# Kernel tuning notes

Measured on AMD Instinct MI355X. Metric: run time of the kernel, lower is better.

The kernel has to match this reference:

```python
import jax, jax.numpy as jnp
import numpy as np

H = 10        # hidden_size
N_TASKS = 5
N_STEPS = 10


def setup_inputs() -> dict:
    key = jax.random.key(0)
    ks = jax.random.split(key, 10)
    omega = jnp.array([0.2, 0.4, 0.6, 0.8, 1.0], dtype=jnp.float32)
    # per-(task, step) human noise: torch.randn(1) * 0.05 each call
    noise = jax.random.normal(ks[0], (N_TASKS, N_STEPS), dtype=jnp.float32) * 0.05
    # h_go1 = randint(0,4,4), h_go2 = randint(4,8,4) -> timestep membership masks
    go1_idx = jax.random.randint(ks[1], (4,), 0, 4)
    go2_idx = jax.random.randint(ks[2], (4,), 4, 8)
    go1_mask = jnp.zeros(N_STEPS, dtype=bool).at[go1_idx].set(True)
    go2_mask = jnp.zeros(N_STEPS, dtype=bool).at[go2_idx].set(True)

    def p(k, shape, fan_in):
        return jax.random.normal(k, shape, dtype=jnp.float32) / jnp.sqrt(jnp.float32(fan_in))

    W_ih = p(ks[3], (4 * H, 2), 2)      # LSTM input weights (gate order i,f,g,o)
    W_hh = p(ks[4], (4 * H, H), H)      # LSTM recurrent weights
    b_ih = p(ks[5], (4 * H,), H)
    b_hh = p(ks[6], (4 * H,), H)
    w1 = p(ks[7], (2 * H, H), H)
    b1 = jnp.zeros(2 * H, jnp.float32)
    w2 = p(ks[8], (2 * H, 2 * H), 2 * H)
    b2 = jnp.zeros(2 * H, jnp.float32)
    w3 = p(ks[9], (1, 2 * H), 2 * H)
    b3 = jnp.zeros(1, jnp.float32)
    return dict(omega=omega, noise=noise, go1_mask=go1_mask, go2_mask=go2_mask,
                W_ih=W_ih, W_hh=W_hh, b_ih=b_ih, b_hh=b_hh,
                w1=w1, b1=b1, w2=w2, b2=b2, w3=w3, b3=b3)


def reference(omega, noise, go1_mask, go2_mask, W_ih, W_hh, b_ih, b_hh,
              w1, b1, w2, b2, w3, b3):
    # human(): branch on s_star in {0.4, 0.8} -> go1 / scale 0.2, else go2 / scale 0.4
    is_g1 = jnp.isclose(omega, 0.4) | jnp.isclose(omega, 0.8)          # [T]
    scale = jnp.where(is_g1, 0.2, 0.4)                                  # [T]
    tmask = jnp.where(is_g1[:, None], go1_mask[None, :], go2_mask[None, :])  # [T,S]
    ah = jnp.where(tmask, (omega - 0.6)[:, None] / scale[:, None], 0.0) + noise  # [T,S]

    def step(carry, ah_t):
        s, h, c, err = carry                       # s:[T], h,c:[T,H], err:[T]
        x = jnp.stack([s, ah_t], axis=-1)          # context = cat(s, ah) -> [T,2]
        gates = x @ W_ih.T + h @ W_hh.T + (b_ih + b_hh)   # [T,4H]
        i, f, g, o = jnp.split(gates, 4, axis=-1)
        i = jax.nn.sigmoid(i); f = jax.nn.sigmoid(f)
        g = jnp.tanh(g);       o = jax.nn.sigmoid(o)
        c = f * c + i * g
        h = o * jnp.tanh(c)
        h1 = jax.nn.relu(h @ w1.T + b1)
        h2 = jax.nn.relu(h1 @ w2.T + b2)
        ar = (h2 @ w3.T + b3)[:, 0]                # robot action [T]
        s = s + ar
        err = err + (s - omega) ** 2
        return (s, h, c, err), None

    init = (jnp.zeros(N_TASKS, jnp.float32),
            jnp.zeros((N_TASKS, H), jnp.float32),
            jnp.zeros((N_TASKS, H), jnp.float32),
            jnp.zeros(N_TASKS, jnp.float32))
    (s, h, c, err), _ = jax.lax.scan(step, init, ah.T)   # scan over the 10 steps
    return jnp.sum(err)    # Q = sum over the 5 tasks of per-rollout squared error
```

## Files before the change

kernel.cpp:

```cpp
#include <hip/hip_runtime.h>

#define HID 10
#define NT 5
#define NS 10

__device__ __forceinline__ float sigf(float x) {
    return 1.0f / (1.0f + __expf(-x));
}
__device__ __forceinline__ float tanh_fast(float x) {
    return 2.0f / (1.0f + __expf(-2.0f * x)) - 1.0f;
}

__device__ __forceinline__ unsigned decode_mask(const void* p) {
    const unsigned* pu = (const unsigned*)p;
    const unsigned char* pb = (const unsigned char*)p;
    unsigned mi = 0, mf = 0, mb = 0;
    bool oki = true, okf = true;
#pragma unroll
    for (int i = 0; i < NS; ++i) {
        unsigned v = pu[i];
        if (v == 1u) mi |= (1u << i);
        else if (v != 0u) oki = false;
        if (v == 0x3F800000u) mf |= (1u << i);
        else if (v != 0u) okf = false;
        if (pb[i]) mb |= (1u << i);
    }
    return oki ? mi : (okf ? mf : mb);
}

__global__ __launch_bounds__(64, 1) void rnnae_kernel(
    const float* __restrict__ omega, const float* __restrict__ noise,
    const void* __restrict__ go1, const void* __restrict__ go2,
    const float* __restrict__ W_ih, const float* __restrict__ W_hh,
    const float* __restrict__ b_ih, const float* __restrict__ b_hh,
    const float* __restrict__ w1, const float* __restrict__ b1,
    const float* __restrict__ w2, const float* __restrict__ b2,
    const float* __restrict__ w3, const float* __restrict__ b3,
    float* __restrict__ out)
{
    const int lane = (int)threadIdx.x;
    float err = 0.0f;

    if (lane < NT * HID) {
        const int t = lane / HID;
        const int u = lane - t * HID;
        const int grp = t * HID;

        const unsigned m1 = decode_mask(go1);
        const unsigned m2 = decode_mask(go2);

        const float om = omega[t];
        const bool is_g1 = (fabsf(om - 0.4f) < 1e-4f) || (fabsf(om - 0.8f) < 1e-4f);
        const float scale = is_g1 ? 0.2f : 0.4f;
        const unsigned msk = is_g1 ? m1 : m2;
        const float base = (om - 0.6f) / scale;

        float ah[NS];
#pragma unroll
        for (int st = 0; st < NS; ++st)
            ah[st] = (((msk >> st) & 1u) ? base : 0.0f) + noise[t * NS + st];

        float wih0[4], wih1[4], whh[4][HID], bg[4];
#pragma unroll
        for (int g = 0; g < 4; ++g) {
            const int r = g * HID + u;
            wih0[g] = W_ih[r * 2 + 0];
            wih1[g] = W_ih[r * 2 + 1];
            bg[g]   = b_ih[r] + b_hh[r];
#pragma unroll
            for (int j = 0; j < HID; ++j) whh[g][j] = W_hh[r * HID + j];
        }
        float w1a[HID], w1b[HID];
#pragma unroll
        for (int j = 0; j < HID; ++j) {
            w1a[j] = w1[u * HID + j];
            w1b[j] = w1[(u + HID) * HID + j];
        }
        const float b1a = b1[u], b1b = b1[u + HID];
        float w2a[2 * HID], w2b[2 * HID];
#pragma unroll
        for (int k = 0; k < 2 * HID; ++k) {
            w2a[k] = w2[u * 2 * HID + k];
            w2b[k] = w2[(u + HID) * 2 * HID + k];
        }
        const float b2a = b2[u], b2b = b2[u + HID];
        const float w3u  = w3[u];
        const float w3uh = w3[u + HID];
        const float b3v  = b3[0];

        float s = 0.0f, c = 0.0f;
        float hj[HID];
#pragma unroll
        for (int j = 0; j < HID; ++j) hj[j] = 0.0f;

#pragma unroll
        for (int st = 0; st < NS; ++st) {
            float acc[4];
#pragma unroll
            for (int g = 0; g < 4; ++g) {
                float a = bg[g] + wih0[g] * s + wih1[g] * ah[st];
#pragma unroll
                for (int j = 0; j < HID; ++j) a += whh[g][j] * hj[j];
                acc[g] = a;
            }
            const float ig = sigf(acc[0]);
            const float fg = sigf(acc[1]);
            const float gg = tanh_fast(acc[2]);
            const float og = sigf(acc[3]);
            c = fg * c + ig * gg;
            const float h = og * tanh_fast(c);

#pragma unroll
            for (int j = 0; j < HID; ++j) hj[j] = __shfl(h, grp + j);

            float x1a = b1a, x1b = b1b;
#pragma unroll
            for (int j = 0; j < HID; ++j) {
                x1a += w1a[j] * hj[j];
                x1b += w1b[j] * hj[j];
            }
            const float h1a = fmaxf(x1a, 0.0f);
            const float h1b = fmaxf(x1b, 0.0f);

            float h1v[2 * HID];
#pragma unroll
            for (int j = 0; j < HID; ++j) {
                h1v[j]       = __shfl(h1a, grp + j);
                h1v[j + HID] = __shfl(h1b, grp + j);
            }
            float x2a = b2a, x2b = b2b;
#pragma unroll
            for (int k = 0; k < 2 * HID; ++k) {
                x2a += w2a[k] * h1v[k];
                x2b += w2b[k] * h1v[k];
            }
            const float h2a = fmaxf(x2a, 0.0f);
            const float h2b = fmaxf(x2b, 0.0f);

            const float pa = w3u * h2a + w3uh * h2b;
            float ar = b3v;
#pragma unroll
            for (int j = 0; j < HID; ++j) ar += __shfl(pa, grp + j);

            s += ar;
            const float d = s - om;
            err += d * d;
        }
    }

    float tot = 0.0f;
#pragma unroll
    for (int t = 0; t < NT; ++t) tot += __shfl(err, t * HID);
    if (lane == 0) out[0] = tot;
}

extern "C" void kernel_launch(void* const* d_in, const int* in_sizes, int n_in,
                              void* d_out, int out_size, void* d_ws, size_t ws_size,
                              hipStream_t stream) {
    rnnae_kernel<<<1, 64, 0, stream>>>(
        (const float*)d_in[0],
        (const float*)d_in[1],
        d_in[2],
        d_in[3],
        (const float*)d_in[4],
        (const float*)d_in[5],
        (const float*)d_in[6],
        (const float*)d_in[7],
        (const float*)d_in[8],
        (const float*)d_in[9],
        (const float*)d_in[10],
        (const float*)d_in[11],
        (const float*)d_in[12],
        (const float*)d_in[13],
        (float*)d_out);
}
```

Before: 89.36 us.

## Rewrite LSTM rollout with 16-lane groups, DPP rotations and LDS weight tables

Each task now occupies a 16-lane DPP row across a 128-thread block. Matvecs use a rotate-and-accumulate scheme: row_ror DPP moves hidden values between lanes, and weights pre-permuted into shared-memory tables are indexed by rotation. The layers are restructured so h feeds both the next-step gate preactivations and the first MLP layer in a single pass, and the final reduction uses DPP butterflies. The aim is to replace the many __shfl (ds_bpermute) ops and large per-lane register weight arrays on the serial critical path with cheaper DPP ops. The cost is a second wave, LDS table setup with a __syncthreads, a non-unrolled step loop and zero-padded work.

```diff
diff --git a/kernel.cpp b/kernel.cpp
--- a/kernel.cpp
+++ b/kernel.cpp
@@ -28,7 +28,12 @@
     return oki ? mi : (okf ? mf : mb);
 }
 
-__global__ __launch_bounds__(64, 1) void rnnae_kernel(
+#define DPPI(x, CTRL) __builtin_amdgcn_update_dpp(0, (x), (CTRL), 0xF, 0xF, true)
+#define ROTF(x, J) __int_as_float( DPPI(__float_as_int(x), 0x110 + (J)) \
+                                 | DPPI(__float_as_int(x), 0x100 + (16 - (J))) )
+#define BFLY(x, CTRL) __int_as_float(DPPI(__float_as_int(x), (CTRL)))
+
+__global__ __launch_bounds__(128, 1) void rnnae_kernel(
     const float* __restrict__ omega, const float* __restrict__ noise,
     const void* __restrict__ go1, const void* __restrict__ go2,
     const float* __restrict__ W_ih, const float* __restrict__ W_hh,
@@ -38,126 +43,149 @@
     const float* __restrict__ w3, const float* __restrict__ b3,
     float* __restrict__ out)
 {
-    const int lane = (int)threadIdx.x;
-    float err = 0.0f;
-
-    if (lane < NT * HID) {
-        const int t = lane / HID;
-        const int u = lane - t * HID;
-        const int grp = t * HID;
-
-        const unsigned m1 = decode_mask(go1);
-        const unsigned m2 = decode_mask(go2);
-
-        const float om = omega[t];
-        const bool is_g1 = (fabsf(om - 0.4f) < 1e-4f) || (fabsf(om - 0.8f) < 1e-4f);
-        const float scale = is_g1 ? 0.2f : 0.4f;
-        const unsigned msk = is_g1 ? m1 : m2;
-        const float base = (om - 0.6f) / scale;
-
-        float ah[NS];
+    const int tid = (int)threadIdx.x;
+    const int t = tid >> 4;
+    const int u = tid & 15;
+    const bool valid = (t < NT);
+
+    __shared__ float4 tabA[16][16];
+    __shared__ float2 tabB[16][16];
+    __shared__ float4 tabC[16][16];
+    __shared__ float terr[NT];
+
 #pragma unroll
-        for (int st = 0; st < NS; ++st)
-            ah[st] = (((msk >> st) & 1u) ? base : 0.0f) + noise[t * NS + st];
-
-        float wih0[4], wih1[4], whh[4][HID], bg[4];
-#pragma unroll
-        for (int g = 0; g < 4; ++g) {
-            const int r = g * HID + u;
-            wih0[g] = W_ih[r * 2 + 0];
-            wih1[g] = W_ih[r * 2 + 1];
-            bg[g]   = b_ih[r] + b_hh[r];
-#pragma unroll
-            for (int j = 0; j < HID; ++j) whh[g][j] = W_hh[r * HID + j];
-        }
-        float w1a[HID], w1b[HID];
-#pragma unroll
-        for (int j = 0; j < HID; ++j) {
-            w1a[j] = w1[u * HID + j];
-            w1b[j] = w1[(u + HID) * HID + j];
-        }
-        const float b1a = b1[u], b1b = b1[u + HID];
-        float w2a[2 * HID], w2b[2 * HID];
-#pragma unroll
-        for (int k = 0; k < 2 * HID; ++k) {
-            w2a[k] = w2[u * 2 * HID + k];
-            w2b[k] = w2[(u + HID) * 2 * HID + k];
-        }
-        const float b2a = b2[u], b2b = b2[u + HID];
-        const float w3u  = w3[u];
-        const float w3uh = w3[u + HID];
-        const float b3v  = b3[0];
-
-        float s = 0.0f, c = 0.0f;
-        float hj[HID];
-#pragma unroll
-        for (int j = 0; j < HID; ++j) hj[j] = 0.0f;
-
-#pragma unroll
-        for (int st = 0; st < NS; ++st) {
-            float acc[4];
-#pragma unroll
-            for (int g = 0; g < 4; ++g) {
-                float a = bg[g] + wih0[g] * s + wih1[g] * ah[st];
-#pragma unroll
-                for (int j = 0; j < HID; ++j) a += whh[g][j] * hj[j];
-                acc[g] = a;
-            }
-            const float ig = sigf(acc[0]);
-            const float fg = sigf(acc[1]);
-            const float gg = tanh_fast(acc[2]);
-            const float og = sigf(acc[3]);
-            c = fg * c + ig * gg;
-            const float h = og * tanh_fast(c);
-
-#pragma unroll
-            for (int j = 0; j < HID; ++j) hj[j] = __shfl(h, grp + j);
-
-            float x1a = b1a, x1b = b1b;
-#pragma unroll
-            for (int j = 0; j < HID; ++j) {
-                x1a += w1a[j] * hj[j];
-                x1b += w1b[j] * hj[j];
-            }
-            const float h1a = fmaxf(x1a, 0.0f);
-            const float h1b = fmaxf(x1b, 0.0f);
-
-            float h1v[2 * HID];
-#pragma unroll
-            for (int j = 0; j < HID; ++j) {
-                h1v[j]       = __shfl(h1a, grp + j);
-                h1v[j + HID] = __shfl(h1b, grp + j);
-            }
-            float x2a = b2a, x2b = b2b;
-#pragma unroll
-            for (int k = 0; k < 2 * HID; ++k) {
-                x2a += w2a[k] * h1v[k];
-                x2b += w2b[k] * h1v[k];
-            }
-            const float h2a = fmaxf(x2a, 0.0f);
-            const float h2b = fmaxf(x2b, 0.0f);
-
-            const float pa = w3u * h2a + w3uh * h2b;
-            float ar = b3v;
-#pragma unroll
-            for (int j = 0; j < HID; ++j) ar += __shfl(pa, grp + j);
-
-            s += ar;
-            const float d = s - om;
-            err += d * d;
-        }
+    for (int p = 0; p < 2; ++p) {
+        const int pair = tid + p * 128;
+        const int j = pair >> 4;
+        const int w = pair & 15;
+        const int idx = (w - j) & 15;
+        const bool hv = (w < HID) && (idx < HID);
+        float4 wa;
+        wa.x = hv ? W_hh[(0 * HID + w) * HID + idx] : 0.0f;
+        wa.y = hv ? W_hh[(1 * HID + w) * HID + idx] : 0.0f;
+        wa.z = hv ? W_hh[(2 * HID + w) * HID + idx] : 0.0f;
+        wa.w = hv ? W_hh[(3 * HID + w) * HID + idx] : 0.0f;
+        tabA[j][w] = wa;
+        float2 wb;
+        wb.x = (idx < HID) ? w1[w * HID + idx] : 0.0f;
+        wb.y = (w < 4 && idx < HID) ? w1[(16 + w) * HID + idx] : 0.0f;
+        tabB[j][w] = wb;
+        float4 wc;
+        wc.x = w2[w * 2 * HID + idx];
+        wc.y = (idx < 4) ? w2[w * 2 * HID + 16 + idx] : 0.0f;
+        wc.z = (w < 4) ? w2[(16 + w) * 2 * HID + idx] : 0.0f;
+        wc.w = (w < 4 && idx < 4) ? w2[(16 + w) * 2 * HID + 16 + idx] : 0.0f;
+        tabC[j][w] = wc;
     }
 
-    float tot = 0.0f;
-#pragma unroll
-    for (int t = 0; t < NT; ++t) tot += __shfl(err, t * HID);
-    if (lane == 0) out[0] = tot;
+    const unsigned m1 = decode_mask(go1);
+    const unsigned m2 = decode_mask(go2);
+    const float om = valid ? omega[t] : 0.0f;
+    const bool is_g1 = (fabsf(om - 0.4f) < 1e-4f) || (fabsf(om - 0.8f) < 1e-4f);
+    const float scale = is_g1 ? 0.2f : 0.4f;
+    const unsigned msk = is_g1 ? m1 : m2;
+    const float base = (om - 0.6f) / scale;
+
+    const bool gv = valid && (u < HID);
+    const float wihs0 = gv ? W_ih[(0 * HID + u) * 2 + 0] : 0.0f;
+    const float wiha0 = gv ? W_ih[(0 * HID + u) * 2 + 1] : 0.0f;
+    const float wihs1 = gv ? W_ih[(1 * HID + u) * 2 + 0] : 0.0f;
+    const float wiha1 = gv ? W_ih[(1 * HID + u) * 2 + 1] : 0.0f;
+    const float wihs2 = gv ? W_ih[(2 * HID + u) * 2 + 0] : 0.0f;
+    const float wiha2 = gv ? W_ih[(2 * HID + u) * 2 + 1] : 0.0f;
+    const float wihs3 = gv ? W_ih[(3 * HID + u) * 2 + 0] : 0.0f;
+    const float wiha3 = gv ? W_ih[(3 * HID + u) * 2 + 1] : 0.0f;
+    const float bgi = gv ? (b_ih[0 * HID + u] + b_hh[0 * HID + u]) : 0.0f;
+    const float bgf = gv ? (b_ih[1 * HID + u] + b_hh[1 * HID + u]) : 0.0f;
+    const float bgg = gv ? (b_ih[2 * HID + u] + b_hh[2 * HID + u]) : 0.0f;
+    const float bgo = gv ? (b_ih[3 * HID + u] + b_hh[3 * HID + u]) : 0.0f;
+    const float b1a = valid ? b1[u] : 0.0f;
+    const float b1b = (valid && u < 4) ? b1[16 + u] : 0.0f;
+    const float b2a = valid ? b2[u] : 0.0f;
+    const float b2b = (valid && u < 4) ? b2[16 + u] : 0.0f;
+    const float w3a = valid ? w3[u] : 0.0f;
+    const float w3b = (valid && u < 4) ? w3[16 + u] : 0.0f;
+    const float b3v = b3[0];
+
+    __syncthreads();
+
+    float s = 0.0f, c = 0.0f, h = 0.0f, err = 0.0f;
+    float hn0 = 0.0f, hn1 = 0.0f, hn2 = 0.0f, hn3 = 0.0f;
+    float nz = valid ? noise[t * NS] : 0.0f;
+
+#pragma unroll 1
+    for (int st = 0; st < NS; ++st) {
+        const float ahv = (((msk >> st) & 1u) ? base : 0.0f) + nz;
+        const int stn = (st < NS - 1) ? st + 1 : st;
+        nz = valid ? noise[t * NS + stn] : 0.0f;
+
+        const float a0 = hn0 + bgi + wihs0 * s + wiha0 * ahv;
+        const float a1 = hn1 + bgf + wihs1 * s + wiha1 * ahv;
+        const float a2 = hn2 + bgg + wihs2 * s + wiha2 * ahv;
+        const float a3 = hn3 + bgo + wihs3 * s + wiha3 * ahv;
+        const float ig = sigf(a0);
+        const float fg = sigf(a1);
+        const float gg = tanh_fast(a2);
+        const float og = sigf(a3);
+        c = fmaf(fg, c, ig * gg);
+        h = og * tanh_fast(c);
+
+        float x1a = b1a, x1b = b1b;
+        hn0 = hn1 = hn2 = hn3 = 0.0f;
+#define S1(J, RV) { const float r_ = (RV); \
+        const float4 wa_ = tabA[J][u]; const float2 wb_ = tabB[J][u]; \
+        hn0 = fmaf(wa_.x, r_, hn0); hn1 = fmaf(wa_.y, r_, hn1); \
+        hn2 = fmaf(wa_.z, r_, hn2); hn3 = fmaf(wa_.w, r_, hn3); \
+        x1a = fmaf(wb_.x, r_, x1a); x1b = fmaf(wb_.y, r_, x1b); }
+        S1(0, h)
+        S1(1,  ROTF(h, 1))  S1(2,  ROTF(h, 2))  S1(3,  ROTF(h, 3))
+        S1(4,  ROTF(h, 4))  S1(5,  ROTF(h, 5))  S1(6,  ROTF(h, 6))
+        S1(7,  ROTF(h, 7))  S1(8,  ROTF(h, 8))  S1(9,  ROTF(h, 9))
+        S1(10, ROTF(h, 10)) S1(11, ROTF(h, 11)) S1(12, ROTF(h, 12))
+        S1(13, ROTF(h, 13)) S1(14, ROTF(h, 14)) S1(15, ROTF(h, 15))
+
+        const float h1a = fmaxf(x1a, 0.0f);
+        const float h1b = fmaxf(x1b, 0.0f);
+
+        float x2a = b2a, x2b = b2b;
+#define S2(J, RA, RB) { const float ra_ = (RA), rb_ = (RB); \
+        const float4 wc_ = tabC[J][u]; \
+        x2a = fmaf(wc_.x, ra_, x2a); x2a = fmaf(wc_.y, rb_, x2a); \
+        x2b = fmaf(wc_.z, ra_, x2b); x2b = fmaf(wc_.w, rb_, x2b); }
+        S2(0, h1a, h1b)
+        S2(1,  ROTF(h1a, 1),  ROTF(h1b, 1))  S2(2,  ROTF(h1a, 2),  ROTF(h1b, 2))
+        S2(3,  ROTF(h1a, 3),  ROTF(h1b, 3))  S2(4,  ROTF(h1a, 4),  ROTF(h1b, 4))
+        S2(5,  ROTF(h1a, 5),  ROTF(h1b, 5))  S2(6,  ROTF(h1a, 6),  ROTF(h1b, 6))
+        S2(7,  ROTF(h1a, 7),  ROTF(h1b, 7))  S2(8,  ROTF(h1a, 8),  ROTF(h1b, 8))
+        S2(9,  ROTF(h1a, 9),  ROTF(h1b, 9))  S2(10, ROTF(h1a, 10), ROTF(h1b, 10))
+        S2(11, ROTF(h1a, 11), ROTF(h1b, 11)) S2(12, ROTF(h1a, 12), ROTF(h1b, 12))
+        S2(13, ROTF(h1a, 13), ROTF(h1b, 13)) S2(14, ROTF(h1a, 14), ROTF(h1b, 14))
+        S2(15, ROTF(h1a, 15), ROTF(h1b, 15))
+
+        const float h2a = fmaxf(x2a, 0.0f);
+        const float h2b = fmaxf(x2b, 0.0f);
+
+        float red = fmaf(w3a, h2a, w3b * h2b);
+        red += BFLY(red, 0xB1);
+        red += BFLY(red, 0x4E);
+        red += BFLY(red, 0x141);
+        red += BFLY(red, 0x140);
+
+        s += red + b3v;
+        const float d = s - om;
+        err = fmaf(d, d, err);
+    }
+
+    if (valid && u == 0) terr[t] = err;
+    __syncthreads();
+    if (tid == 0)
+        out[0] = terr[0] + terr[1] + terr[2] + terr[3] + terr[4];
 }
 
 extern "C" void kernel_launch(void* const* d_in, const int* in_sizes, int n_in,
                               void* d_out, int out_size, void* d_ws, size_t ws_size,
                               hipStream_t stream) {
-    rnnae_kernel<<<1, 64, 0, stream>>>(
+    rnnae_kernel<<<1, 128, 0, stream>>>(
         (const float*)d_in[0],
         (const float*)d_in[1],
         d_in[2],
```

Measured after the change: 88.37 us. Within noise of the previous version (-1.1%).
